# Kernel tuning notes

Hardware: AMD Instinct MI355X
Metric: run time of the kernel (lower is better)

The kernel has to match this reference:

```python
import jax, jax.numpy as jnp
import numpy as np

V, E, H, C, T = 50000, 512, 1024, 1221, 4096


def setup_inputs() -> dict:
    key = jax.random.key(0)
    ks = jax.random.split(key, 8)
    s = 1.0 / np.sqrt(H)  # PyTorch LSTM/Linear init scale
    return {
        "x": jax.random.randint(ks[0], (T,), 0, V),
        "emb_table": jax.random.normal(ks[1], (V, E), jnp.float32),
        "W_ih": jax.random.uniform(ks[2], (4 * H, 2 * E), jnp.float32, -s, s),
        "W_hh": jax.random.uniform(ks[3], (4 * H, H), jnp.float32, -s, s),
        "b_ih": jax.random.uniform(ks[4], (4 * H,), jnp.float32, -s, s),
        "b_hh": jax.random.uniform(ks[5], (4 * H,), jnp.float32, -s, s),
        "W_out": jax.random.uniform(ks[6], (C, H), jnp.float32, -s, s),
        "b_out": jax.random.uniform(ks[7], (C,), jnp.float32, -s, s),
    }


def reference(x, emb_table, W_ih, W_hh, b_ih, b_hh, W_out, b_out):
    emb = emb_table[x]                       # [T, E]
    last = emb[-1]                           # [E] embedding of final token
    n = emb.shape[0] - 1
    # each step input: concat(word_i, word_last) -> [T-1, 2E]
    xs = jnp.concatenate(
        [emb[:-1], jnp.broadcast_to(last, (n, last.shape[0]))], axis=1
    )
    # Precompute input projections for all steps in one GEMM: [T-1, 4H]
    x_gates = xs @ W_ih.T + b_ih + b_hh
    hdim = W_hh.shape[1]

    def step(carry, xg):
        h, c = carry
        gates = xg + h @ W_hh.T              # [4H], PyTorch gate order i,f,g,o
        i, f, g, o = jnp.split(gates, 4)
        i = jax.nn.sigmoid(i)
        f = jax.nn.sigmoid(f)
        g = jnp.tanh(g)
        o = jax.nn.sigmoid(o)
        c = f * c + i * g
        h = o * jnp.tanh(c)
        return (h, c), h

    h0 = jnp.zeros((hdim,), dtype=x_gates.dtype)
    c0 = jnp.zeros((hdim,), dtype=x_gates.dtype)
    _, hs = jax.lax.scan(step, (h0, c0), x_gates)  # hs: [T-1, H]
    out = hs @ W_out.T + b_out                     # [T-1, C]
    return out[None, :, :]                         # (1, T-1, C)
```

## Files before the change

### kernel.cpp

```cpp
#include <hip/hip_runtime.h>
#include <math.h>

#define NSTEP 4095
#define EDIM  512
#define HDIM  1024
#define GDIM  4096
#define KDIM  1024
#define CDIM  1221
#define SNWG  64
#define UNITS 16

#define PIN4(v) asm volatile("" : "+v"((v).x), "+v"((v).y), "+v"((v).z), "+v"((v).w))

__device__ __forceinline__ float sigmoidf_(float v) {
    return 1.0f / (1.0f + __expf(-v));
}
__device__ __forceinline__ float tanhf_(float v) {
    v = fminf(fmaxf(v, -15.0f), 15.0f);
    const float e2 = __expf(2.0f * v);
    return (e2 - 1.0f) / (e2 + 1.0f);
}

__global__ __launch_bounds__(256) void gemm_emb_kernel(
    const int* __restrict__ x, const float* __restrict__ emb,
    const float* __restrict__ W, const float* __restrict__ b_ih,
    const float* __restrict__ b_hh, float* __restrict__ xg)
{
    __shared__ float As[8][128];
    __shared__ float Bs[8][128];
    const int tid = threadIdx.x;
    const int bm = blockIdx.y * 128, bn = blockIdx.x * 128;
    const int tx = tid & 15, ty = tid >> 4;
    const int lrow = tid >> 1;
    const int lk4  = (tid & 1) * 4;
    const int lastTok = x[NSTEP];
    const int am = bm + lrow;
    const int tokRow = (am < NSTEP) ? x[am] : 0;
    const int bnrow = bn + lrow;

    float acc[8][8];
#pragma unroll
    for (int i = 0; i < 8; ++i)
#pragma unroll
        for (int j = 0; j < 8; ++j) acc[i][j] = 0.0f;

    for (int k0 = 0; k0 < KDIM; k0 += 8) {
        const int k = k0 + lk4;
        float4 av = make_float4(0.f, 0.f, 0.f, 0.f);
        if (am < NSTEP) {
            const int tok = (k < EDIM) ? tokRow : lastTok;
            const int kk  = (k < EDIM) ? k : (k - EDIM);
            av = *(const float4*)(emb + (size_t)tok * EDIM + kk);
        }
        const float4 bv = *(const float4*)(W + (size_t)bnrow * KDIM + k);
        __syncthreads();
        As[lk4 + 0][lrow] = av.x; As[lk4 + 1][lrow] = av.y;
        As[lk4 + 2][lrow] = av.z; As[lk4 + 3][lrow] = av.w;
        Bs[lk4 + 0][lrow] = bv.x; Bs[lk4 + 1][lrow] = bv.y;
        Bs[lk4 + 2][lrow] = bv.z; Bs[lk4 + 3][lrow] = bv.w;
        __syncthreads();
#pragma unroll
        for (int kk = 0; kk < 8; ++kk) {
            const float4 a0 = *(const float4*)&As[kk][ty * 4];
            const float4 a1 = *(const float4*)&As[kk][ty * 4 + 64];
            const float4 b0 = *(const float4*)&Bs[kk][tx * 4];
            const float4 b1 = *(const float4*)&Bs[kk][tx * 4 + 64];
            const float a[8] = {a0.x, a0.y, a0.z, a0.w, a1.x, a1.y, a1.z, a1.w};
            const float b[8] = {b0.x, b0.y, b0.z, b0.w, b1.x, b1.y, b1.z, b1.w};
#pragma unroll
            for (int i = 0; i < 8; ++i)
#pragma unroll
                for (int j = 0; j < 8; ++j) acc[i][j] += a[i] * b[j];
        }
    }
#pragma unroll
    for (int i = 0; i < 8; ++i) {
        const int m = bm + ((i < 4) ? (ty * 4 + i) : (64 + ty * 4 + i - 4));
        if (m >= NSTEP) continue;
#pragma unroll
        for (int j = 0; j < 8; ++j) {
            const int n = bn + ((j < 4) ? (tx * 4 + j) : (64 + tx * 4 + j - 4));
            xg[(size_t)m * GDIM + n] = acc[i][j] + b_ih[n] + b_hh[n];
        }
    }
}

__global__ __launch_bounds__(256) void gemm_out_kernel(
    const float* __restrict__ A, const float* __restrict__ W,
    const float* __restrict__ bias, float* __restrict__ C)
{
    __shared__ float As[8][128];
    __shared__ float Bs[8][128];
    const int tid = threadIdx.x;
    const int bm = blockIdx.y * 128, bn = blockIdx.x * 128;
    const int tx = tid & 15, ty = tid >> 4;
    const int lrow = tid >> 1;
    const int lk4  = (tid & 1) * 4;
    const int am = bm + lrow;
    const int bnrow = bn + lrow;

    float acc[8][8];
#pragma unroll
    for (int i = 0; i < 8; ++i)
#pragma unroll
        for (int j = 0; j < 8; ++j) acc[i][j] = 0.0f;

    for (int k0 = 0; k0 < KDIM; k0 += 8) {
        const int k = k0 + lk4;
        float4 av = make_float4(0.f, 0.f, 0.f, 0.f);
        if (am < NSTEP) av = *(const float4*)(A + (size_t)am * KDIM + k);
        float4 bv = make_float4(0.f, 0.f, 0.f, 0.f);
        if (bnrow < CDIM) bv = *(const float4*)(W + (size_t)bnrow * KDIM + k);
        __syncthreads();
        As[lk4 + 0][lrow] = av.x; As[lk4 + 1][lrow] = av.y;
        As[lk4 + 2][lrow] = av.z; As[lk4 + 3][lrow] = av.w;
        Bs[lk4 + 0][lrow] = bv.x; Bs[lk4 + 1][lrow] = bv.y;
        Bs[lk4 + 2][lrow] = bv.z; Bs[lk4 + 3][lrow] = bv.w;
        __syncthreads();
#pragma unroll
        for (int kk = 0; kk < 8; ++kk) {
            const float4 a0 = *(const float4*)&As[kk][ty * 4];
            const float4 a1 = *(const float4*)&As[kk][ty * 4 + 64];
            const float4 b0 = *(const float4*)&Bs[kk][tx * 4];
            const float4 b1 = *(const float4*)&Bs[kk][tx * 4 + 64];
            const float a[8] = {a0.x, a0.y, a0.z, a0.w, a1.x, a1.y, a1.z, a1.w};
            const float b[8] = {b0.x, b0.y, b0.z, b0.w, b1.x, b1.y, b1.z, b1.w};
#pragma unroll
            for (int i = 0; i < 8; ++i)
#pragma unroll
                for (int j = 0; j < 8; ++j) acc[i][j] += a[i] * b[j];
        }
    }
#pragma unroll
    for (int i = 0; i < 8; ++i) {
        const int m = bm + ((i < 4) ? (ty * 4 + i) : (64 + ty * 4 + i - 4));
        if (m >= NSTEP) continue;
#pragma unroll
        for (int j = 0; j < 8; ++j) {
            const int n = bn + ((j < 4) ? (tx * 4 + j) : (64 + tx * 4 + j - 4));
            if (n < CDIM) C[(size_t)m * CDIM + n] = acc[i][j] + bias[n];
        }
    }
}

__global__ __launch_bounds__(1024, 4) void scan_kernel(
    const float* __restrict__ xg, const float* __restrict__ Whh,
    float* __restrict__ hs, unsigned long long* hb)
{
    __shared__ float h_s[HDIM];
    __shared__ float gate_s[64];
    __shared__ float c_s[UNITS];
    const int g = blockIdx.x, tid = threadIdx.x;
    const int lane = tid & 63, wv = tid >> 6;
    const int seg = tid & 15, lr = tid >> 4;
    const int q = lr >> 4, j = lr & 15;
    const int grow = q * HDIM + g * UNITS + j;

    float4 w4[16];
#pragma unroll
    for (int i = 0; i < 16; ++i)
        w4[i] = *(const float4*)(Whh + (size_t)grow * KDIM + i * 64 + seg * 4);

    for (int i = tid; i < HDIM; i += 1024) h_s[i] = 0.0f;
    if (tid < UNITS) c_s[tid] = 0.0f;
    __syncthreads();

    for (int t = 1; t <= NSTEP; ++t) {
#pragma unroll
        for (int i = 0; i < 16; ++i) PIN4(w4[i]);

        float xgv = 0.0f;
        if (seg == 0) xgv = xg[(size_t)(t - 1) * GDIM + grow];

        if (t > 1) {
            const int par = (t - 1) & 1;
            const int el = wv * 64 + lane;
            const int want = t - 1;
            unsigned long long v;
            for (;;) {
                v = __hip_atomic_load(&hb[par * HDIM + el], __ATOMIC_RELAXED,
                                      __HIP_MEMORY_SCOPE_AGENT);
                if ((int)(v >> 32) == want) break;
            }
            h_s[el] = __uint_as_float((unsigned)v);
        }
        __syncthreads();

        float acc = 0.0f;
#pragma unroll
        for (int i = 0; i < 16; ++i) {
            const float4 h4 = *(const float4*)&h_s[i * 64 + seg * 4];
            acc += w4[i].x * h4.x + w4[i].y * h4.y +
                   w4[i].z * h4.z + w4[i].w * h4.w;
        }
        acc += __shfl_xor(acc, 1, 64);
        acc += __shfl_xor(acc, 2, 64);
        acc += __shfl_xor(acc, 4, 64);
        acc += __shfl_xor(acc, 8, 64);
        if (seg == 0) gate_s[lr] = acc + xgv;
        __syncthreads();

        if (tid < UNITS) {
            const int jj = tid;
            const float ig = sigmoidf_(gate_s[jj]);
            const float fg = sigmoidf_(gate_s[16 + jj]);
            const float gg = tanhf_(gate_s[32 + jj]);
            const float og = sigmoidf_(gate_s[48 + jj]);
            const float c  = fg * c_s[jj] + ig * gg;
            c_s[jj] = c;
            const float h = og * tanhf_(c);
            hs[(size_t)(t - 1) * HDIM + g * UNITS + jj] = h;
            const unsigned long long pv =
                ((unsigned long long)(unsigned)t << 32) | __float_as_uint(h);
            __hip_atomic_store(&hb[(t & 1) * HDIM + g * UNITS + jj], pv,
                               __ATOMIC_RELAXED, __HIP_MEMORY_SCOPE_AGENT);
        }
    }
}

extern "C" void kernel_launch(void* const* d_in, const int* in_sizes, int n_in,
                              void* d_out, int out_size, void* d_ws, size_t ws_size,
                              hipStream_t stream)
{
    const int*   x     = (const int*)d_in[0];
    const float* emb   = (const float*)d_in[1];
    const float* W_ih  = (const float*)d_in[2];
    const float* W_hh  = (const float*)d_in[3];
    const float* b_ih  = (const float*)d_in[4];
    const float* b_hh  = (const float*)d_in[5];
    const float* W_out = (const float*)d_in[6];
    const float* b_out = (const float*)d_in[7];
    float* out = (float*)d_out;

    float* xg = (float*)d_ws;
    float* hs = xg + (size_t)NSTEP * GDIM;
    unsigned long long* hb =
        (unsigned long long*)(hs + (size_t)NSTEP * HDIM);

    dim3 blk(256);
    dim3 g1(GDIM / 128, 32);
    gemm_emb_kernel<<<g1, blk, 0, stream>>>(x, emb, W_ih, b_ih, b_hh, xg);

    scan_kernel<<<dim3(SNWG), dim3(1024), 0, stream>>>(xg, W_hh, hs, hb);

    dim3 g2((CDIM + 127) / 128, 32);
    gemm_out_kernel<<<g2, blk, 0, stream>>>(hs, W_out, b_out, out);
}
```

Before: 8.367 ms.

## Map one LSTM unit per wavefront and drop second barrier in recurrent scan

Reassigns threads so that each wavefront owns one hidden unit, with the four gate rows held in its four 16-lane quarters. Gate values are gathered with wave shuffles and the cell state stays in a register, which removes the gate_s shared buffer and the second __syncthreads per step. h_s becomes double-buffered by step parity so the one remaining barrier is enough. The register-pinning asm on the weights is also removed, which may let the compiler spill or reload them.

```diff
diff --git a/kernel.cpp b/kernel.cpp
--- a/kernel.cpp
+++ b/kernel.cpp
@@ -9,8 +9,6 @@
 #define CDIM  1221
 #define SNWG  64
 #define UNITS 16
-
-#define PIN4(v) asm volatile("" : "+v"((v).x), "+v"((v).y), "+v"((v).z), "+v"((v).w))
 
 __device__ __forceinline__ float sigmoidf_(float v) {
     return 1.0f / (1.0f + __expf(-v));
@@ -147,49 +145,45 @@
     const float* __restrict__ xg, const float* __restrict__ Whh,
     float* __restrict__ hs, unsigned long long* hb)
 {
-    __shared__ float h_s[HDIM];
-    __shared__ float gate_s[64];
-    __shared__ float c_s[UNITS];
+    __shared__ float h_s[2][HDIM];
     const int g = blockIdx.x, tid = threadIdx.x;
-    const int lane = tid & 63, wv = tid >> 6;
-    const int seg = tid & 15, lr = tid >> 4;
-    const int q = lr >> 4, j = lr & 15;
-    const int grow = q * HDIM + g * UNITS + j;
+    const int w = tid >> 6, lane = tid & 63;
+    const int q = lane >> 4, seg = lane & 15;
+    const int unit = g * UNITS + w;
+    const int grow = q * HDIM + unit;
 
     float4 w4[16];
 #pragma unroll
     for (int i = 0; i < 16; ++i)
         w4[i] = *(const float4*)(Whh + (size_t)grow * KDIM + i * 64 + seg * 4);
 
-    for (int i = tid; i < HDIM; i += 1024) h_s[i] = 0.0f;
-    if (tid < UNITS) c_s[tid] = 0.0f;
+    for (int i = tid; i < 2 * HDIM; i += 1024) ((float*)h_s)[i] = 0.0f;
     __syncthreads();
 
+    float c = 0.0f;
+
     for (int t = 1; t <= NSTEP; ++t) {
-#pragma unroll
-        for (int i = 0; i < 16; ++i) PIN4(w4[i]);
+        const int par = (t - 1) & 1;
 
         float xgv = 0.0f;
         if (seg == 0) xgv = xg[(size_t)(t - 1) * GDIM + grow];
 
         if (t > 1) {
-            const int par = (t - 1) & 1;
-            const int el = wv * 64 + lane;
             const int want = t - 1;
             unsigned long long v;
             for (;;) {
-                v = __hip_atomic_load(&hb[par * HDIM + el], __ATOMIC_RELAXED,
+                v = __hip_atomic_load(&hb[par * HDIM + tid], __ATOMIC_RELAXED,
                                       __HIP_MEMORY_SCOPE_AGENT);
                 if ((int)(v >> 32) == want) break;
             }
-            h_s[el] = __uint_as_float((unsigned)v);
-        }
-        __syncthreads();
-
-        float acc = 0.0f;
+            h_s[par][tid] = __uint_as_float((unsigned)v);
+        }
+        __syncthreads();
+
+        float acc = (seg == 0) ? xgv : 0.0f;
 #pragma unroll
         for (int i = 0; i < 16; ++i) {
-            const float4 h4 = *(const float4*)&h_s[i * 64 + seg * 4];
+            const float4 h4 = *(const float4*)&h_s[par][i * 64 + seg * 4];
             acc += w4[i].x * h4.x + w4[i].y * h4.y +
                    w4[i].z * h4.z + w4[i].w * h4.w;
         }
@@ -197,22 +191,23 @@
         acc += __shfl_xor(acc, 2, 64);
         acc += __shfl_xor(acc, 4, 64);
         acc += __shfl_xor(acc, 8, 64);
-        if (seg == 0) gate_s[lr] = acc + xgv;
-        __syncthreads();
-
-        if (tid < UNITS) {
-            const int jj = tid;
-            const float ig = sigmoidf_(gate_s[jj]);
-            const float fg = sigmoidf_(gate_s[16 + jj]);
-            const float gg = tanhf_(gate_s[32 + jj]);
-            const float og = sigmoidf_(gate_s[48 + jj]);
-            const float c  = fg * c_s[jj] + ig * gg;
-            c_s[jj] = c;
-            const float h = og * tanhf_(c);
-            hs[(size_t)(t - 1) * HDIM + g * UNITS + jj] = h;
+        const float g0 = __shfl(acc,  0, 64);
+        const float g1 = __shfl(acc, 16, 64);
+        const float g2 = __shfl(acc, 32, 64);
+        const float g3 = __shfl(acc, 48, 64);
+
+        const float ig = sigmoidf_(g0);
+        const float fg = sigmoidf_(g1);
+        const float gg = tanhf_(g2);
+        const float og = sigmoidf_(g3);
+        c = fg * c + ig * gg;
+        const float h = og * tanhf_(c);
+
+        if (lane == 0) {
+            hs[(size_t)(t - 1) * HDIM + unit] = h;
             const unsigned long long pv =
                 ((unsigned long long)(unsigned)t << 32) | __float_as_uint(h);
-            __hip_atomic_store(&hb[(t & 1) * HDIM + g * UNITS + jj], pv,
+            __hip_atomic_store(&hb[(t & 1) * HDIM + unit], pv,
                                __ATOMIC_RELAXED, __HIP_MEMORY_SCOPE_AGENT);
         }
     }
```

Result: slower. 16.20 ms (+93.6%).
